# Kernel tuning notes

Hardware: AMD Instinct MI355X
Metric: run time of the kernel (lower is better)

Reference implementation:

```python
import jax, jax.numpy as jnp
import numpy as np

B, S, H, L, O = 128, 2048, 128, 2, 2  # batch, seq, hidden(=input), layers, output


def setup_inputs() -> dict:
    key = jax.random.key(0)
    k1, k2, k3, k4, k5 = jax.random.split(key, 5)
    std = 1.0 / np.sqrt(H)
    x_data = jax.random.normal(k1, (B, S, H), dtype=jnp.float32)
    x_length = jax.random.randint(k2, (B,), 0, S, dtype=jnp.int32)
    x_label = jax.random.uniform(k3, (B,), dtype=jnp.float32)
    # torch Linear layout: y = x @ W.T ; init uniform(-1/sqrt(H), 1/sqrt(H))
    Wx2h = jax.random.uniform(k4, (L, 2 * H, H), minval=-std, maxval=std, dtype=jnp.float32)
    Wfc = jax.random.uniform(k5, (L, O, H), minval=-std, maxval=std, dtype=jnp.float32)
    return {"x_data": x_data, "x_length": x_length, "x_label": x_label,
            "Wx2h": Wx2h, "Wfc": Wfc}


def reference(x_data, x_length, x_label, Wx2h, Wfc):
    Bn, Sn, Hn = x_data.shape
    Ln = Wx2h.shape[0]
    # valid-timestep mask: seq index < x_length[i]
    mask = (jnp.arange(Sn)[None, :] < x_length[:, None]).astype(x_data.dtype)  # [B,S]

    def step(carry, inp):
        S1, S2 = carry            # each [L,B,H]
        x_t, m_t = inp            # [B,H], [B]
        h = x_t
        out = None
        S1_new, S2_new = [], []
        for l in range(Ln):
            gate = h @ Wx2h[l].T                    # [B,2H]
            m1, m2 = jnp.split(gate, 2, axis=1)
            s1n = S1[l] + jnp.tanh(m1)
            s2n = S2[l] + jnp.tanh(m2)
            Fu = jax.nn.relu(s1n)
            h = (1.0 - Fu) * s2n + Fu * S2[l]       # hy
            out = jax.nn.softmax(h @ Wfc[l].T, axis=1)  # [B,O]
            S1_new.append(s1n)
            S2_new.append(s2n)
        loss_t = m_t * (x_label - jax.nn.sigmoid(out[:, 1])) ** 2  # [B]
        return (jnp.stack(S1_new), jnp.stack(S2_new)), loss_t

    S0 = jnp.zeros((Ln, Bn, Hn), x_data.dtype)
    xs = (jnp.swapaxes(x_data, 0, 1), mask.T)  # time-major [S,B,H], [S,B]
    _, losses = jax.lax.scan(step, (S0, S0), xs)
    return jnp.sum(losses)
```

## Files before the change

kernel.cpp:

```cpp
#include <hip/hip_runtime.h>

typedef __bf16 bf16;
typedef __bf16 bf16x8 __attribute__((ext_vector_type(8)));
typedef float floatx4 __attribute__((ext_vector_type(4)));

#define BATCH 128
#define SEQ   2048
#define HID   128
#define TWOH  256
#define CH    128
#define NCH   16
#define MTOT  (BATCH * SEQ)

__device__ __forceinline__ float fast_tanh(float x) {
    float e = __builtin_amdgcn_exp2f(2.88539008177793f * x);
    return 1.0f - 2.0f * __builtin_amdgcn_rcpf(e + 1.0f);
}
__device__ __forceinline__ float fast_sigmoid(float x) {
    return __builtin_amdgcn_rcpf(1.0f + __builtin_amdgcn_exp2f(-1.44269504088896f * x));
}

union PK4 { unsigned long long u; bf16 h[4]; };

__global__ __launch_bounds__(256) void convert_w_k(const float* __restrict__ W,
                                                   bf16* __restrict__ Wb) {
    int i = blockIdx.x * 256 + threadIdx.x;
    float4 v = ((const float4*)W)[i];
    PK4 pk;
    pk.h[0] = (bf16)v.x; pk.h[1] = (bf16)v.y;
    pk.h[2] = (bf16)v.z; pk.h[3] = (bf16)v.w;
    ((unsigned long long*)Wb)[i] = pk.u;
}

template <int MODE, bool AF32>
__global__ __launch_bounds__(512, 4) void fused_k(const void* __restrict__ Aptr,
                                                  const bf16* __restrict__ Wb,
                                                  const float* __restrict__ Pbase,
                                                  float* __restrict__ Pout,
                                                  bf16* __restrict__ Hb,
                                                  const float* __restrict__ Wfc,
                                                  const int* __restrict__ xlen,
                                                  const float* __restrict__ xlab,
                                                  float* __restrict__ out) {
    __shared__ bf16 As[128 * 128];
    __shared__ bf16 Bs[128 * 128];
    __shared__ float aux[512];
    __shared__ float zbuf[4][128][2];
    __shared__ float red[2];

    const int tid  = threadIdx.x;
    const int lane = tid & 63;
    const int wid  = tid >> 6;
    const int wr   = wid >> 2;
    const int wc   = wid & 3;
    const int quad = lane >> 4;
    const int l16  = lane & 15;
    const long blk = blockIdx.x;
    const long rowBase = blk * 128;

    if (AF32) {
        const float4* A4 = (const float4*)((const float*)Aptr + rowBase * HID);
        #pragma unroll
        for (int it = 0; it < 8; ++it) {
            int i  = it * 512 + tid;
            int r  = i >> 5;
            int c4 = i & 31;
            float4 v = A4[i];
            int g = c4 >> 1, hf = c4 & 1;
            PK4 pk;
            pk.h[0] = (bf16)v.x; pk.h[1] = (bf16)v.y;
            pk.h[2] = (bf16)v.z; pk.h[3] = (bf16)v.w;
            *(unsigned long long*)&As[r * 128 + ((g ^ (r & 7)) << 3) + (hf << 2)] = pk.u;
        }
    } else {
        const uint4* A8 = (const uint4*)((const bf16*)Aptr + rowBase * HID);
        #pragma unroll
        for (int it = 0; it < 4; ++it) {
            int i = it * 512 + tid;
            int r = i >> 4;
            int g = i & 15;
            uint4 v = A8[i];
            *(uint4*)&As[r * 128 + ((g ^ (r & 7)) << 3)] = v;
        }
    }

    float p1[4][2][4];

    #pragma unroll
    for (int half = 0; half < 2; ++half) {
        __syncthreads();
        {
            const uint4* W8 = (const uint4*)(Wb + half * 128 * HID);
            #pragma unroll
            for (int it = 0; it < 4; ++it) {
                int i = it * 512 + tid;
                int r = i >> 4;
                int g = i & 15;
                uint4 v = W8[i];
                *(uint4*)&Bs[r * 128 + ((g ^ (r & 7)) << 3)] = v;
            }
        }
        __syncthreads();

        floatx4 acc[4][2];
        #pragma unroll
        for (int a = 0; a < 4; ++a)
            #pragma unroll
            for (int b2 = 0; b2 < 2; ++b2) acc[a][b2] = (floatx4){0.f, 0.f, 0.f, 0.f};

        #pragma unroll
        for (int kk = 0; kk < 128; kk += 32) {
            bf16x8 af[4], bfr[2];
            int kg = (kk >> 3) + quad;
            #pragma unroll
            for (int mi = 0; mi < 4; ++mi) {
                int r = wr * 64 + mi * 16 + l16;
                af[mi] = *(const bf16x8*)&As[r * 128 + ((kg ^ (r & 7)) << 3)];
            }
            #pragma unroll
            for (int ni = 0; ni < 2; ++ni) {
                int n = wc * 32 + ni * 16 + l16;
                bfr[ni] = *(const bf16x8*)&Bs[n * 128 + ((kg ^ (n & 7)) << 3)];
            }
            #pragma unroll
            for (int mi = 0; mi < 4; ++mi)
                #pragma unroll
                for (int ni = 0; ni < 2; ++ni)
                    acc[mi][ni] = __builtin_amdgcn_mfma_f32_16x16x32_bf16(
                        af[mi], bfr[ni], acc[mi][ni], 0, 0, 0);
        }

        float g2[4][2][4];
        #pragma unroll
        for (int mi = 0; mi < 4; ++mi)
            #pragma unroll
            for (int ni = 0; ni < 2; ++ni)
                #pragma unroll
                for (int rr = 0; rr < 4; ++rr)
                    g2[mi][ni][rr] = fast_tanh(acc[mi][ni][rr]);

        if (MODE == 0) {
            #pragma unroll
            for (int ni = 0; ni < 2; ++ni) {
                float cs = 0.f;
                #pragma unroll
                for (int mi = 0; mi < 4; ++mi)
                    #pragma unroll
                    for (int rr = 0; rr < 4; ++rr) cs += g2[mi][ni][rr];
                cs += __shfl_xor(cs, 16);
                cs += __shfl_xor(cs, 32);
                if (quad == 0)
                    aux[wr * 256 + half * 128 + wc * 32 + ni * 16 + l16] = cs;
            }
        } else {
            float pref[4][2][4];
            #pragma unroll
            for (int ni = 0; ni < 2; ++ni) {
                float mibase = 0.f;
                #pragma unroll
                for (int mi = 0; mi < 4; ++mi) {
                    float s0 = g2[mi][ni][0];
                    float s1 = s0 + g2[mi][ni][1];
                    float s2 = s1 + g2[mi][ni][2];
                    float s3 = s2 + g2[mi][ni][3];
                    float tot = s3;
                    float xq = tot;
                    float t = __shfl_up(xq, 16);
                    if (quad >= 1) xq += t;
                    t = __shfl_up(xq, 32);
                    if (quad >= 2) xq += t;
                    float excl = mibase + xq - tot;
                    pref[mi][ni][0] = excl + s0;
                    pref[mi][ni][1] = excl + s1;
                    pref[mi][ni][2] = excl + s2;
                    pref[mi][ni][3] = excl + s3;
                    mibase += __shfl(xq, 48 + l16);
                }
                if (wr == 0 && quad == 0)
                    aux[wc * 32 + ni * 16 + l16] = mibase;
            }
            __syncthreads();

            if (half == 0) {
                #pragma unroll
                for (int ni = 0; ni < 2; ++ni) {
                    int col = wc * 32 + ni * 16 + l16;
                    float off = Pbase[(blk << 8) + col];
                    if (wr) off += aux[col];
                    #pragma unroll
                    for (int mi = 0; mi < 4; ++mi)
                        #pragma unroll
                        for (int rr = 0; rr < 4; ++rr)
                            p1[mi][ni][rr] = pref[mi][ni][rr] + off;
                }
            } else {
                if (MODE == 1) {
                    #pragma unroll
                    for (int ni = 0; ni < 2; ++ni) {
                        int col = wc * 32 + ni * 16 + l16;
                        float off = Pbase[(blk << 8) + 128 + col];
                        if (wr) off += aux[col];
                        #pragma unroll
                        for (int mi = 0; mi < 4; ++mi)
                            #pragma unroll
                            for (int rr = 0; rr < 4; ++rr) {
                                long row = rowBase + wr * 64 + mi * 16 + quad * 4 + rr;
                                float h = pref[mi][ni][rr] + off -
                                          fmaxf(p1[mi][ni][rr], 0.f) * g2[mi][ni][rr];
                                Hb[row * HID + col] = (bf16)h;
                            }
                    }
                } else {
                    float w0[2], w1[2], off[2];
                    #pragma unroll
                    for (int ni = 0; ni < 2; ++ni) {
                        int col = wc * 32 + ni * 16 + l16;
                        w0[ni] = Wfc[2 * HID + col];
                        w1[ni] = Wfc[3 * HID + col];
                        off[ni] = Pbase[(blk << 8) + 128 + col];
                        if (wr) off[ni] += aux[col];
                    }
                    #pragma unroll
                    for (int mi = 0; mi < 4; ++mi)
                        #pragma unroll
                        for (int rr = 0; rr < 4; ++rr) {
                            float z0 = 0.f, z1 = 0.f;
                            #pragma unroll
                            for (int ni = 0; ni < 2; ++ni) {
                                float h = pref[mi][ni][rr] + off[ni] -
                                          fmaxf(p1[mi][ni][rr], 0.f) * g2[mi][ni][rr];
                                z0 += h * w0[ni];
                                z1 += h * w1[ni];
                            }
                            z0 += __shfl_xor(z0, 1); z1 += __shfl_xor(z1, 1);
                            z0 += __shfl_xor(z0, 2); z1 += __shfl_xor(z1, 2);
                            z0 += __shfl_xor(z0, 4); z1 += __shfl_xor(z1, 4);
                            z0 += __shfl_xor(z0, 8); z1 += __shfl_xor(z1, 8);
                            if (l16 == 0) {
                                int row = wr * 64 + mi * 16 + quad * 4 + rr;
                                zbuf[wc][row][0] = z0;
                                zbuf[wc][row][1] = z1;
                            }
                        }
                }
            }
        }
    }

    if (MODE == 0) {
        __syncthreads();
        if (tid < 256) Pout[(blk << 8) + tid] = aux[tid] + aux[256 + tid];
    } else if (MODE == 2) {
        __syncthreads();
        float lsum = 0.f;
        if (tid < 128) {
            int row = tid;
            int b = (int)(blk >> 4), chunk = (int)(blk & 15);
            float z0 = zbuf[0][row][0] + zbuf[1][row][0] + zbuf[2][row][0] + zbuf[3][row][0];
            float z1 = zbuf[0][row][1] + zbuf[1][row][1] + zbuf[2][row][1] + zbuf[3][row][1];
            float o1 = fast_sigmoid(z1 - z0);
            float sg = fast_sigmoid(o1);
            float d = xlab[b] - sg;
            if (chunk * CH + row < xlen[b]) lsum = d * d;
            lsum += __shfl_xor(lsum, 1);
            lsum += __shfl_xor(lsum, 2);
            lsum += __shfl_xor(lsum, 4);
            lsum += __shfl_xor(lsum, 8);
            lsum += __shfl_xor(lsum, 16);
            lsum += __shfl_xor(lsum, 32);
            if (lane == 0) red[wid] = lsum;
        }
        __syncthreads();
        if (tid == 0) atomicAdd(out, red[0] + red[1]);
    }
}

__global__ __launch_bounds__(256) void scan_partials_k(float* __restrict__ P) {
    int ch = threadIdx.x;
    long b = blockIdx.x;
    float v[NCH];
    #pragma unroll
    for (int c = 0; c < NCH; ++c) v[c] = P[((b * NCH + c) << 8) + ch];
    float run = 0.f;
    #pragma unroll
    for (int c = 0; c < NCH; ++c) {
        float t = v[c];
        P[((b * NCH + c) << 8) + ch] = run;
        run += t;
    }
}

extern "C" void kernel_launch(void* const* d_in, const int* in_sizes, int n_in,
                              void* d_out, int out_size, void* d_ws, size_t ws_size,
                              hipStream_t stream) {
    const float* x    = (const float*)d_in[0];
    const int*   xlen = (const int*)d_in[1];
    const float* xlab = (const float*)d_in[2];
    const float* Wx2h = (const float*)d_in[3];
    const float* Wfc  = (const float*)d_in[4];
    float* out = (float*)d_out;

    char* ws = (char*)d_ws;
    bf16*  Hb = (bf16*)ws;
    float* P  = (float*)(ws + (size_t)MTOT * HID * 2);
    bf16*  Wb = (bf16*)((char*)P + (size_t)BATCH * NCH * TWOH * 4);

    hipMemsetAsync(d_out, 0, sizeof(float), stream);
    convert_w_k<<<64, 256, 0, stream>>>(Wx2h, Wb);

    fused_k<0, true><<<MTOT / 128, 512, 0, stream>>>(x, Wb, nullptr, P, nullptr,
                                                     nullptr, nullptr, nullptr, nullptr);
    scan_partials_k<<<BATCH, 256, 0, stream>>>(P);
    fused_k<1, true><<<MTOT / 128, 512, 0, stream>>>(x, Wb, P, nullptr, Hb,
                                                     nullptr, nullptr, nullptr, nullptr);
    fused_k<0, false><<<MTOT / 128, 512, 0, stream>>>(Hb, Wb + TWOH * HID, nullptr, P,
                                                      nullptr, nullptr, nullptr, nullptr, nullptr);
    scan_partials_k<<<BATCH, 256, 0, stream>>>(P);
    fused_k<2, false><<<MTOT / 128, 512, 0, stream>>>(Hb, Wb + TWOH * HID, P, nullptr,
                                                      nullptr, Wfc, xlen, xlab, out);
}
```

Baseline: 375.7 us.

## Store tanh gate tiles instead of recomputing GEMMs; fuse layer-1 input build

```diff
diff --git a/kernel.cpp b/kernel.cpp
--- a/kernel.cpp
+++ b/kernel.cpp
@@ -21,6 +21,7 @@
 }
 
 union PK4 { unsigned long long u; bf16 h[4]; };
+union PK8 { uint4 u; bf16 h[8]; };
 
 __global__ __launch_bounds__(256) void convert_w_k(const float* __restrict__ W,
                                                    bf16* __restrict__ Wb) {
@@ -32,21 +33,38 @@
     ((unsigned long long*)Wb)[i] = pk.u;
 }
 
-template <int MODE, bool AF32>
-__global__ __launch_bounds__(512, 4) void fused_k(const void* __restrict__ Aptr,
-                                                  const bf16* __restrict__ Wb,
-                                                  const float* __restrict__ Pbase,
-                                                  float* __restrict__ Pout,
-                                                  bf16* __restrict__ Hb,
-                                                  const float* __restrict__ Wfc,
-                                                  const int* __restrict__ xlen,
-                                                  const float* __restrict__ xlab,
-                                                  float* __restrict__ out) {
+__device__ __forceinline__ void tile_prefix(const float g[4][4], float pref[4][4],
+                                            float* stripe_tot, int quad, int l16) {
+    float mibase = 0.f;
+    #pragma unroll
+    for (int mi = 0; mi < 4; ++mi) {
+        float s0 = g[mi][0];
+        float s1 = s0 + g[mi][1];
+        float s2 = s1 + g[mi][2];
+        float s3 = s2 + g[mi][3];
+        float tot = s3, xq = tot;
+        float t = __shfl_up(xq, 16);
+        if (quad >= 1) xq += t;
+        t = __shfl_up(xq, 32);
+        if (quad >= 2) xq += t;
+        float excl = mibase + xq - tot;
+        pref[mi][0] = excl + s0;
+        pref[mi][1] = excl + s1;
+        pref[mi][2] = excl + s2;
+        pref[mi][3] = excl + s3;
+        mibase += __shfl(xq, 48 + l16);
+    }
+    *stripe_tot = mibase;
+}
+
+
+__global__ __launch_bounds__(512, 4) void l0_k(const float* __restrict__ x,
+                                               const bf16* __restrict__ Wb,
+                                               uint4* __restrict__ T,
+                                               float* __restrict__ Pout) {
     __shared__ bf16 As[128 * 128];
     __shared__ bf16 Bs[128 * 128];
-    __shared__ float aux[512];
-    __shared__ float zbuf[4][128][2];
-    __shared__ float red[2];
+    __shared__ float psum[512];
 
     const int tid  = threadIdx.x;
     const int lane = tid & 63;
@@ -58,8 +76,8 @@
     const long blk = blockIdx.x;
     const long rowBase = blk * 128;
 
-    if (AF32) {
-        const float4* A4 = (const float4*)((const float*)Aptr + rowBase * HID);
+    {
+        const float4* A4 = (const float4*)(x + rowBase * HID);
         #pragma unroll
         for (int it = 0; it < 8; ++it) {
             int i  = it * 512 + tid;
@@ -72,25 +90,13 @@
             pk.h[2] = (bf16)v.z; pk.h[3] = (bf16)v.w;
             *(unsigned long long*)&As[r * 128 + ((g ^ (r & 7)) << 3) + (hf << 2)] = pk.u;
         }
-    } else {
-        const uint4* A8 = (const uint4*)((const bf16*)Aptr + rowBase * HID);
-        #pragma unroll
-        for (int it = 0; it < 4; ++it) {
-            int i = it * 512 + tid;
-            int r = i >> 4;
-            int g = i & 15;
-            uint4 v = A8[i];
-            *(uint4*)&As[r * 128 + ((g ^ (r & 7)) << 3)] = v;
-        }
-    }
-
-    float p1[4][2][4];
+    }
 
     #pragma unroll
     for (int half = 0; half < 2; ++half) {
         __syncthreads();
         {
-            const uint4* W8 = (const uint4*)(Wb + half * 128 * HID);
+            const uint4* W8 = (const uint4*)(Wb + (size_t)half * 128 * HID);
             #pragma unroll
             for (int it = 0; it < 4; ++it) {
                 int i = it * 512 + tid;
@@ -130,149 +136,42 @@
                         af[mi], bfr[ni], acc[mi][ni], 0, 0, 0);
         }
 
-        float g2[4][2][4];
+        float g2[2][4][4];
         #pragma unroll
         for (int mi = 0; mi < 4; ++mi)
             #pragma unroll
             for (int ni = 0; ni < 2; ++ni)
                 #pragma unroll
                 for (int rr = 0; rr < 4; ++rr)
-                    g2[mi][ni][rr] = fast_tanh(acc[mi][ni][rr]);
-
-        if (MODE == 0) {
-            #pragma unroll
-            for (int ni = 0; ni < 2; ++ni) {
-                float cs = 0.f;
-                #pragma unroll
-                for (int mi = 0; mi < 4; ++mi)
-                    #pragma unroll
-                    for (int rr = 0; rr < 4; ++rr) cs += g2[mi][ni][rr];
-                cs += __shfl_xor(cs, 16);
-                cs += __shfl_xor(cs, 32);
-                if (quad == 0)
-                    aux[wr * 256 + half * 128 + wc * 32 + ni * 16 + l16] = cs;
-            }
-        } else {
-            float pref[4][2][4];
-            #pragma unroll
-            for (int ni = 0; ni < 2; ++ni) {
-                float mibase = 0.f;
-                #pragma unroll
-                for (int mi = 0; mi < 4; ++mi) {
-                    float s0 = g2[mi][ni][0];
-                    float s1 = s0 + g2[mi][ni][1];
-                    float s2 = s1 + g2[mi][ni][2];
-                    float s3 = s2 + g2[mi][ni][3];
-                    float tot = s3;
-                    float xq = tot;
-                    float t = __shfl_up(xq, 16);
-                    if (quad >= 1) xq += t;
-                    t = __shfl_up(xq, 32);
-                    if (quad >= 2) xq += t;
-                    float excl = mibase + xq - tot;
-                    pref[mi][ni][0] = excl + s0;
-                    pref[mi][ni][1] = excl + s1;
-                    pref[mi][ni][2] = excl + s2;
-                    pref[mi][ni][3] = excl + s3;
-                    mibase += __shfl(xq, 48 + l16);
-                }
-                if (wr == 0 && quad == 0)
-                    aux[wc * 32 + ni * 16 + l16] = mibase;
-            }
-            __syncthreads();
-
-            if (half == 0) {
-                #pragma unroll
-                for (int ni = 0; ni < 2; ++ni) {
-                    int col = wc * 32 + ni * 16 + l16;
-                    float off = Pbase[(blk << 8) + col];
-                    if (wr) off += aux[col];
-                    #pragma unroll
-                    for (int mi = 0; mi < 4; ++mi)
-                        #pragma unroll
-                        for (int rr = 0; rr < 4; ++rr)
-                            p1[mi][ni][rr] = pref[mi][ni][rr] + off;
-                }
-            } else {
-                if (MODE == 1) {
-                    #pragma unroll
-                    for (int ni = 0; ni < 2; ++ni) {
-                        int col = wc * 32 + ni * 16 + l16;
-                        float off = Pbase[(blk << 8) + 128 + col];
-                        if (wr) off += aux[col];
-                        #pragma unroll
-                        for (int mi = 0; mi < 4; ++mi)
-                            #pragma unroll
-                            for (int rr = 0; rr < 4; ++rr) {
-                                long row = rowBase + wr * 64 + mi * 16 + quad * 4 + rr;
-                                float h = pref[mi][ni][rr] + off -
-                                          fmaxf(p1[mi][ni][rr], 0.f) * g2[mi][ni][rr];
-                                Hb[row * HID + col] = (bf16)h;
-                            }
-                    }
-                } else {
-                    float w0[2], w1[2], off[2];
-                    #pragma unroll
-                    for (int ni = 0; ni < 2; ++ni) {
-                        int col = wc * 32 + ni * 16 + l16;
-                        w0[ni] = Wfc[2 * HID + col];
-                        w1[ni] = Wfc[3 * HID + col];
-                        off[ni] = Pbase[(blk << 8) + 128 + col];
-                        if (wr) off[ni] += aux[col];
-                    }
-                    #pragma unroll
-                    for (int mi = 0; mi < 4; ++mi)
-                        #pragma unroll
-                        for (int rr = 0; rr < 4; ++rr) {
-                            float z0 = 0.f, z1 = 0.f;
-                            #pragma unroll
-                            for (int ni = 0; ni < 2; ++ni) {
-                                float h = pref[mi][ni][rr] + off[ni] -
-                                          fmaxf(p1[mi][ni][rr], 0.f) * g2[mi][ni][rr];
-                                z0 += h * w0[ni];
-                                z1 += h * w1[ni];
-                            }
-                            z0 += __shfl_xor(z0, 1); z1 += __shfl_xor(z1, 1);
-                            z0 += __shfl_xor(z0, 2); z1 += __shfl_xor(z1, 2);
-                            z0 += __shfl_xor(z0, 4); z1 += __shfl_xor(z1, 4);
-                            z0 += __shfl_xor(z0, 8); z1 += __shfl_xor(z1, 8);
-                            if (l16 == 0) {
-                                int row = wr * 64 + mi * 16 + quad * 4 + rr;
-                                zbuf[wc][row][0] = z0;
-                                zbuf[wc][row][1] = z1;
-                            }
-                        }
-                }
-            }
-        }
-    }
-
-    if (MODE == 0) {
-        __syncthreads();
-        if (tid < 256) Pout[(blk << 8) + tid] = aux[tid] + aux[256 + tid];
-    } else if (MODE == 2) {
-        __syncthreads();
-        float lsum = 0.f;
-        if (tid < 128) {
-            int row = tid;
-            int b = (int)(blk >> 4), chunk = (int)(blk & 15);
-            float z0 = zbuf[0][row][0] + zbuf[1][row][0] + zbuf[2][row][0] + zbuf[3][row][0];
-            float z1 = zbuf[0][row][1] + zbuf[1][row][1] + zbuf[2][row][1] + zbuf[3][row][1];
-            float o1 = fast_sigmoid(z1 - z0);
-            float sg = fast_sigmoid(o1);
-            float d = xlab[b] - sg;
-            if (chunk * CH + row < xlen[b]) lsum = d * d;
-            lsum += __shfl_xor(lsum, 1);
-            lsum += __shfl_xor(lsum, 2);
-            lsum += __shfl_xor(lsum, 4);
-            lsum += __shfl_xor(lsum, 8);
-            lsum += __shfl_xor(lsum, 16);
-            lsum += __shfl_xor(lsum, 32);
-            if (lane == 0) red[wid] = lsum;
-        }
-        __syncthreads();
-        if (tid == 0) atomicAdd(out, red[0] + red[1]);
-    }
+                    g2[ni][mi][rr] = fast_tanh(acc[mi][ni][rr]);
+
+        #pragma unroll
+        for (int mi = 0; mi < 4; ++mi) {
+            PK8 p;
+            #pragma unroll
+            for (int rr = 0; rr < 4; ++rr) {
+                p.h[rr]     = (bf16)g2[0][mi][rr];
+                p.h[4 + rr] = (bf16)g2[1][mi][rr];
+            }
+            T[((blk * 2 + half) * 4 + mi) * 512 + tid] = p.u;
+        }
+
+        #pragma unroll
+        for (int ni = 0; ni < 2; ++ni) {
+            float cs = 0.f;
+            #pragma unroll
+            for (int mi = 0; mi < 4; ++mi)
+                #pragma unroll
+                for (int rr = 0; rr < 4; ++rr) cs += g2[ni][mi][rr];
+            cs += __shfl_xor(cs, 16);
+            cs += __shfl_xor(cs, 32);
+            if (quad == 0)
+                psum[wr * 256 + half * 128 + wc * 32 + ni * 16 + l16] = cs;
+        }
+    }
+
+    __syncthreads();
+    if (tid < 256) Pout[(blk << 8) + tid] = psum[tid] + psum[256 + tid];
 }
 
 __global__ __launch_bounds__(256) void scan_partials_k(float* __restrict__ P) {
@@ -290,6 +189,308 @@
     }
 }
 
+__global__ __launch_bounds__(512, 4) void l1_k(const bf16* __restrict__ Wb1,
+                                               uint4* __restrict__ T,
+                                               const float* __restrict__ P0,
+                                               float* __restrict__ Pout) {
+    __shared__ bf16 As[128 * 128];
+    __shared__ bf16 Bs[128 * 128];
+    __shared__ float auxp[128];
+    __shared__ float psum[512];
+
+    const int tid  = threadIdx.x;
+    const int lane = tid & 63;
+    const int wid  = tid >> 6;
+    const int wr   = wid >> 2;
+    const int wc   = wid & 3;
+    const int quad = lane >> 4;
+    const int l16  = lane & 15;
+    const long blk = blockIdx.x;
+
+    float p1[2][4][4];
+
+    {
+        float g2[2][4][4];
+        #pragma unroll
+        for (int mi = 0; mi < 4; ++mi) {
+            PK8 p;
+            p.u = T[((blk * 2 + 0) * 4 + mi) * 512 + tid];
+            #pragma unroll
+            for (int rr = 0; rr < 4; ++rr) {
+                g2[0][mi][rr] = (float)p.h[rr];
+                g2[1][mi][rr] = (float)p.h[4 + rr];
+            }
+        }
+        float pref[2][4][4], st[2];
+        #pragma unroll
+        for (int ni = 0; ni < 2; ++ni) {
+            tile_prefix(g2[ni], pref[ni], &st[ni], quad, l16);
+            if (wr == 0 && quad == 0) auxp[wc * 32 + ni * 16 + l16] = st[ni];
+        }
+        __syncthreads();
+        #pragma unroll
+        for (int ni = 0; ni < 2; ++ni) {
+            int col = wc * 32 + ni * 16 + l16;
+            float off = P0[(blk << 8) + col];
+            if (wr) off += auxp[col];
+            #pragma unroll
+            for (int mi = 0; mi < 4; ++mi)
+                #pragma unroll
+                for (int rr = 0; rr < 4; ++rr)
+                    p1[ni][mi][rr] = pref[ni][mi][rr] + off;
+        }
+    }
+    __syncthreads();
+
+    {
+        float g2[2][4][4];
+        #pragma unroll
+        for (int mi = 0; mi < 4; ++mi) {
+            PK8 p;
+            p.u = T[((blk * 2 + 1) * 4 + mi) * 512 + tid];
+            #pragma unroll
+            for (int rr = 0; rr < 4; ++rr) {
+                g2[0][mi][rr] = (float)p.h[rr];
+                g2[1][mi][rr] = (float)p.h[4 + rr];
+            }
+        }
+        float pref[2][4][4], st[2];
+        #pragma unroll
+        for (int ni = 0; ni < 2; ++ni) {
+            tile_prefix(g2[ni], pref[ni], &st[ni], quad, l16);
+            if (wr == 0 && quad == 0) auxp[wc * 32 + ni * 16 + l16] = st[ni];
+        }
+        __syncthreads();
+        #pragma unroll
+        for (int ni = 0; ni < 2; ++ni) {
+            int col = wc * 32 + ni * 16 + l16;
+            int gsw = col >> 3, rem = col & 7;
+            float off = P0[(blk << 8) + 128 + col];
+            if (wr) off += auxp[col];
+            #pragma unroll
+            for (int mi = 0; mi < 4; ++mi)
+                #pragma unroll
+                for (int rr = 0; rr < 4; ++rr) {
+                    int row = wr * 64 + mi * 16 + quad * 4 + rr;
+                    float h = pref[ni][mi][rr] + off -
+                              fmaxf(p1[ni][mi][rr], 0.f) * g2[ni][mi][rr];
+                    As[row * 128 + ((gsw ^ (row & 7)) << 3) + rem] = (bf16)h;
+                }
+        }
+    }
+
+    #pragma unroll
+    for (int half = 0; half < 2; ++half) {
+        __syncthreads();
+        {
+            const uint4* W8 = (const uint4*)(Wb1 + (size_t)half * 128 * HID);
+            #pragma unroll
+            for (int it = 0; it < 4; ++it) {
+                int i = it * 512 + tid;
+                int r = i >> 4;
+                int g = i & 15;
+                uint4 v = W8[i];
+                *(uint4*)&Bs[r * 128 + ((g ^ (r & 7)) << 3)] = v;
+            }
+        }
+        __syncthreads();
+
+        floatx4 acc[4][2];
+        #pragma unroll
+        for (int a = 0; a < 4; ++a)
+            #pragma unroll
+            for (int b2 = 0; b2 < 2; ++b2) acc[a][b2] = (floatx4){0.f, 0.f, 0.f, 0.f};
+
+        #pragma unroll
+        for (int kk = 0; kk < 128; kk += 32) {
+            bf16x8 af[4], bfr[2];
+            int kg = (kk >> 3) + quad;
+            #pragma unroll
+            for (int mi = 0; mi < 4; ++mi) {
+                int r = wr * 64 + mi * 16 + l16;
+                af[mi] = *(const bf16x8*)&As[r * 128 + ((kg ^ (r & 7)) << 3)];
+            }
+            #pragma unroll
+            for (int ni = 0; ni < 2; ++ni) {
+                int n = wc * 32 + ni * 16 + l16;
+                bfr[ni] = *(const bf16x8*)&Bs[n * 128 + ((kg ^ (n & 7)) << 3)];
+            }
+            #pragma unroll
+            for (int mi = 0; mi < 4; ++mi)
+                #pragma unroll
+                for (int ni = 0; ni < 2; ++ni)
+                    acc[mi][ni] = __builtin_amdgcn_mfma_f32_16x16x32_bf16(
+                        af[mi], bfr[ni], acc[mi][ni], 0, 0, 0);
+        }
+
+        float g2[2][4][4];
+        #pragma unroll
+        for (int mi = 0; mi < 4; ++mi)
+            #pragma unroll
+            for (int ni = 0; ni < 2; ++ni)
+                #pragma unroll
+                for (int rr = 0; rr < 4; ++rr)
+                    g2[ni][mi][rr] = fast_tanh(acc[mi][ni][rr]);
+
+        #pragma unroll
+        for (int mi = 0; mi < 4; ++mi) {
+            PK8 p;
+            #pragma unroll
+            for (int rr = 0; rr < 4; ++rr) {
+                p.h[rr]     = (bf16)g2[0][mi][rr];
+                p.h[4 + rr] = (bf16)g2[1][mi][rr];
+            }
+            T[((blk * 2 + half) * 4 + mi) * 512 + tid] = p.u;
+        }
+
+        #pragma unroll
+        for (int ni = 0; ni < 2; ++ni) {
+            float cs = 0.f;
+            #pragma unroll
+            for (int mi = 0; mi < 4; ++mi)
+                #pragma unroll
+                for (int rr = 0; rr < 4; ++rr) cs += g2[ni][mi][rr];
+            cs += __shfl_xor(cs, 16);
+            cs += __shfl_xor(cs, 32);
+            if (quad == 0)
+                psum[wr * 256 + half * 128 + wc * 32 + ni * 16 + l16] = cs;
+        }
+    }
+
+    __syncthreads();
+    if (tid < 256) Pout[(blk << 8) + tid] = psum[tid] + psum[256 + tid];
+}
+
+__global__ __launch_bounds__(512, 4) void loss_k(const uint4* __restrict__ T,
+                                                 const float* __restrict__ P1,
+                                                 const float* __restrict__ Wfc,
+                                                 const int* __restrict__ xlen,
+                                                 const float* __restrict__ xlab,
+                                                 float* __restrict__ out) {
+    __shared__ float auxp[128];
+    __shared__ float zbuf[4][128][2];
+    __shared__ float red[2];
+
+    const int tid  = threadIdx.x;
+    const int lane = tid & 63;
+    const int wid  = tid >> 6;
+    const int wr   = wid >> 2;
+    const int wc   = wid & 3;
+    const int quad = lane >> 4;
+    const int l16  = lane & 15;
+    const long blk = blockIdx.x;
+
+    float p1[2][4][4];
+
+    {
+        float g2[2][4][4];
+        #pragma unroll
+        for (int mi = 0; mi < 4; ++mi) {
+            PK8 p;
+            p.u = T[((blk * 2 + 0) * 4 + mi) * 512 + tid];
+            #pragma unroll
+            for (int rr = 0; rr < 4; ++rr) {
+                g2[0][mi][rr] = (float)p.h[rr];
+                g2[1][mi][rr] = (float)p.h[4 + rr];
+            }
+        }
+        float pref[2][4][4], st[2];
+        #pragma unroll
+        for (int ni = 0; ni < 2; ++ni) {
+            tile_prefix(g2[ni], pref[ni], &st[ni], quad, l16);
+            if (wr == 0 && quad == 0) auxp[wc * 32 + ni * 16 + l16] = st[ni];
+        }
+        __syncthreads();
+        #pragma unroll
+        for (int ni = 0; ni < 2; ++ni) {
+            int col = wc * 32 + ni * 16 + l16;
+            float off = P1[(blk << 8) + col];
+            if (wr) off += auxp[col];
+            #pragma unroll
+            for (int mi = 0; mi < 4; ++mi)
+                #pragma unroll
+                for (int rr = 0; rr < 4; ++rr)
+                    p1[ni][mi][rr] = pref[ni][mi][rr] + off;
+        }
+    }
+    __syncthreads();
+
+    {
+        float g2[2][4][4];
+        #pragma unroll
+        for (int mi = 0; mi < 4; ++mi) {
+            PK8 p;
+            p.u = T[((blk * 2 + 1) * 4 + mi) * 512 + tid];
+            #pragma unroll
+            for (int rr = 0; rr < 4; ++rr) {
+                g2[0][mi][rr] = (float)p.h[rr];
+                g2[1][mi][rr] = (float)p.h[4 + rr];
+            }
+        }
+        float pref[2][4][4], st[2];
+        #pragma unroll
+        for (int ni = 0; ni < 2; ++ni) {
+            tile_prefix(g2[ni], pref[ni], &st[ni], quad, l16);
+            if (wr == 0 && quad == 0) auxp[wc * 32 + ni * 16 + l16] = st[ni];
+        }
+        __syncthreads();
+
+        float w0[2], w1[2], off[2];
+        #pragma unroll
+        for (int ni = 0; ni < 2; ++ni) {
+            int col = wc * 32 + ni * 16 + l16;
+            w0[ni] = Wfc[2 * HID + col];
+            w1[ni] = Wfc[3 * HID + col];
+            off[ni] = P1[(blk << 8) + 128 + col];
+            if (wr) off[ni] += auxp[col];
+        }
+        #pragma unroll
+        for (int mi = 0; mi < 4; ++mi)
+            #pragma unroll
+            for (int rr = 0; rr < 4; ++rr) {
+                float z0 = 0.f, z1 = 0.f;
+                #pragma unroll
+                for (int ni = 0; ni < 2; ++ni) {
+                    float h = pref[ni][mi][rr] + off[ni] -
+                              fmaxf(p1[ni][mi][rr], 0.f) * g2[ni][mi][rr];
+                    z0 += h * w0[ni];
+                    z1 += h * w1[ni];
+                }
+                z0 += __shfl_xor(z0, 1); z1 += __shfl_xor(z1, 1);
+                z0 += __shfl_xor(z0, 2); z1 += __shfl_xor(z1, 2);
+                z0 += __shfl_xor(z0, 4); z1 += __shfl_xor(z1, 4);
+                z0 += __shfl_xor(z0, 8); z1 += __shfl_xor(z1, 8);
+                if (l16 == 0) {
+                    int row = wr * 64 + mi * 16 + quad * 4 + rr;
+                    zbuf[wc][row][0] = z0;
+                    zbuf[wc][row][1] = z1;
+                }
+            }
+    }
+
+    __syncthreads();
+    float lsum = 0.f;
+    if (tid < 128) {
+        int row = tid;
+        int b = (int)(blk >> 4), chunk = (int)(blk & 15);
+        float z0 = zbuf[0][row][0] + zbuf[1][row][0] + zbuf[2][row][0] + zbuf[3][row][0];
+        float z1 = zbuf[0][row][1] + zbuf[1][row][1] + zbuf[2][row][1] + zbuf[3][row][1];
+        float o1 = fast_sigmoid(z1 - z0);
+        float sg = fast_sigmoid(o1);
+        float d = xlab[b] - sg;
+        if (chunk * CH + row < xlen[b]) lsum = d * d;
+        lsum += __shfl_xor(lsum, 1);
+        lsum += __shfl_xor(lsum, 2);
+        lsum += __shfl_xor(lsum, 4);
+        lsum += __shfl_xor(lsum, 8);
+        lsum += __shfl_xor(lsum, 16);
+        lsum += __shfl_xor(lsum, 32);
+        if (lane == 0) red[wid] = lsum;
+    }
+    __syncthreads();
+    if (tid == 0) atomicAdd(out, red[0] + red[1]);
+}
+
 extern "C" void kernel_launch(void* const* d_in, const int* in_sizes, int n_in,
                               void* d_out, int out_size, void* d_ws, size_t ws_size,
                               hipStream_t stream) {
@@ -301,21 +502,17 @@
     float* out = (float*)d_out;
 
     char* ws = (char*)d_ws;
-    bf16*  Hb = (bf16*)ws;
-    float* P  = (float*)(ws + (size_t)MTOT * HID * 2);
-    bf16*  Wb = (bf16*)((char*)P + (size_t)BATCH * NCH * TWOH * 4);
+    uint4* T  = (uint4*)ws;
+    float* P0 = (float*)(ws + (size_t)MTOT * TWOH * 2);
+    float* P1 = P0 + (size_t)BATCH * NCH * TWOH;
+    bf16*  Wb = (bf16*)(P1 + (size_t)BATCH * NCH * TWOH);
 
     hipMemsetAsync(d_out, 0, sizeof(float), stream);
     convert_w_k<<<64, 256, 0, stream>>>(Wx2h, Wb);
 
-    fused_k<0, true><<<MTOT / 128, 512, 0, stream>>>(x, Wb, nullptr, P, nullptr,
-                                                     nullptr, nullptr, nullptr, nullptr);
-    scan_partials_k<<<BATCH, 256, 0, stream>>>(P);
-    fused_k<1, true><<<MTOT / 128, 512, 0, stream>>>(x, Wb, P, nullptr, Hb,
-                                                     nullptr, nullptr, nullptr, nullptr);
-    fused_k<0, false><<<MTOT / 128, 512, 0, stream>>>(Hb, Wb + TWOH * HID, nullptr, P,
-                                                      nullptr, nullptr, nullptr, nullptr, nullptr);
-    scan_partials_k<<<BATCH, 256, 0, stream>>>(P);
-    fused_k<2, false><<<MTOT / 128, 512, 0, stream>>>(Hb, Wb + TWOH * HID, P, nullptr,
-                                                      nullptr, Wfc, xlen, xlab, out);
-}
+    l0_k<<<MTOT / 128, 512, 0, stream>>>(x, Wb, T, P0);
+    scan_partials_k<<<BATCH, 256, 0, stream>>>(P0);
+    l1_k<<<MTOT / 128, 512, 0, stream>>>(Wb + (size_t)TWOH * HID, T, P0, P1);
+    scan_partials_k<<<BATCH, 256, 0, stream>>>(P1);
+    loss_k<<<MTOT / 128, 512, 0, stream>>>(T, P1, Wfc, xlen, xlab, out);
+}
```

Result: faster. 340.6 us (-9.3%).

## Fuse both layers into one per-batch kernel with sequential chunk scan

Applied to the files above, without the earlier changes.

```diff
diff --git a/kernel.cpp b/kernel.cpp
--- a/kernel.cpp
+++ b/kernel.cpp
@@ -10,7 +10,6 @@
 #define TWOH  256
 #define CH    128
 #define NCH   16
-#define MTOT  (BATCH * SEQ)
 
 __device__ __forceinline__ float fast_tanh(float x) {
     float e = __builtin_amdgcn_exp2f(2.88539008177793f * x);
@@ -32,19 +31,39 @@
     ((unsigned long long*)Wb)[i] = pk.u;
 }
 
-template <int MODE, bool AF32>
-__global__ __launch_bounds__(512, 4) void fused_k(const void* __restrict__ Aptr,
+__device__ __forceinline__ void tile_prefix(const float g[4][4], float pref[4][4],
+                                            float* stripe_tot, int quad, int l16) {
+    float mibase = 0.f;
+    #pragma unroll
+    for (int mi = 0; mi < 4; ++mi) {
+        float s0 = g[mi][0];
+        float s1 = s0 + g[mi][1];
+        float s2 = s1 + g[mi][2];
+        float s3 = s2 + g[mi][3];
+        float tot = s3, xq = tot;
+        float t = __shfl_up(xq, 16);
+        if (quad >= 1) xq += t;
+        t = __shfl_up(xq, 32);
+        if (quad >= 2) xq += t;
+        float excl = mibase + xq - tot;
+        pref[mi][0] = excl + s0;
+        pref[mi][1] = excl + s1;
+        pref[mi][2] = excl + s2;
+        pref[mi][3] = excl + s3;
+        mibase += __shfl(xq, 48 + l16);
+    }
+    *stripe_tot = mibase;
+}
+
+__global__ __launch_bounds__(512, 2) void batch_k(const float* __restrict__ x,
                                                   const bf16* __restrict__ Wb,
-                                                  const float* __restrict__ Pbase,
-                                                  float* __restrict__ Pout,
-                                                  bf16* __restrict__ Hb,
                                                   const float* __restrict__ Wfc,
                                                   const int* __restrict__ xlen,
                                                   const float* __restrict__ xlab,
                                                   float* __restrict__ out) {
     __shared__ bf16 As[128 * 128];
-    __shared__ bf16 Bs[128 * 128];
-    __shared__ float aux[512];
+    __shared__ bf16 Ws[256 * 128];
+    __shared__ float aux[2][2][128];
     __shared__ float zbuf[4][128][2];
     __shared__ float red[2];
 
@@ -55,171 +74,174 @@
     const int wc   = wid & 3;
     const int quad = lane >> 4;
     const int l16  = lane & 15;
-    const long blk = blockIdx.x;
-    const long rowBase = blk * 128;
-
-    if (AF32) {
-        const float4* A4 = (const float4*)((const float*)Aptr + rowBase * HID);
+    const int bb   = blockIdx.x;
+    const int xl   = xlen[bb];
+    const int nact = (xl + CH - 1) >> 7;
+    if (nact == 0) return;
+
+    float wfc0[2], wfc1[2];
+    #pragma unroll
+    for (int ni = 0; ni < 2; ++ni) {
+        int col = wc * 32 + ni * 16 + l16;
+        wfc0[ni] = Wfc[2 * HID + col];
+        wfc1[ni] = Wfc[3 * HID + col];
+    }
+    const float xlb = xlab[bb];
+
+    float offr[2][2][2];
+    #pragma unroll
+    for (int a = 0; a < 2; ++a)
+        #pragma unroll
+        for (int b = 0; b < 2; ++b) { offr[a][b][0] = 0.f; offr[a][b][1] = 0.f; }
+    float lsum = 0.f;
+
+    float4 xr[8];
+    uint4  wreg[8];
+    {
+        const float4* A4 = (const float4*)(x + (size_t)bb * SEQ * HID);
+        #pragma unroll
+        for (int it = 0; it < 8; ++it) xr[it] = A4[it * 512 + tid];
+        const uint4* W8 = (const uint4*)Wb;
+        #pragma unroll
+        for (int it = 0; it < 8; ++it) wreg[it] = W8[it * 512 + tid];
+    }
+
+    for (int c = 0; c < nact; ++c) {
+        __syncthreads();
         #pragma unroll
         for (int it = 0; it < 8; ++it) {
             int i  = it * 512 + tid;
             int r  = i >> 5;
             int c4 = i & 31;
-            float4 v = A4[i];
             int g = c4 >> 1, hf = c4 & 1;
+            float4 v = xr[it];
             PK4 pk;
             pk.h[0] = (bf16)v.x; pk.h[1] = (bf16)v.y;
             pk.h[2] = (bf16)v.z; pk.h[3] = (bf16)v.w;
             *(unsigned long long*)&As[r * 128 + ((g ^ (r & 7)) << 3) + (hf << 2)] = pk.u;
         }
-    } else {
-        const uint4* A8 = (const uint4*)((const bf16*)Aptr + rowBase * HID);
-        #pragma unroll
-        for (int it = 0; it < 4; ++it) {
+        #pragma unroll
+        for (int it = 0; it < 8; ++it) {
             int i = it * 512 + tid;
             int r = i >> 4;
             int g = i & 15;
-            uint4 v = A8[i];
-            *(uint4*)&As[r * 128 + ((g ^ (r & 7)) << 3)] = v;
-        }
-    }
-
-    float p1[4][2][4];
-
-    #pragma unroll
-    for (int half = 0; half < 2; ++half) {
+            *(uint4*)&Ws[r * 128 + ((g ^ (r & 7)) << 3)] = wreg[it];
+        }
+        if (c + 1 < nact) {
+            const float4* A4 =
+                (const float4*)(x + ((size_t)bb * SEQ + (size_t)(c + 1) * CH) * HID);
+            #pragma unroll
+            for (int it = 0; it < 8; ++it) xr[it] = A4[it * 512 + tid];
+        }
+        {
+            const uint4* W8 = (const uint4*)(Wb + (size_t)TWOH * HID);
+            #pragma unroll
+            for (int it = 0; it < 8; ++it) wreg[it] = W8[it * 512 + tid];
+        }
         __syncthreads();
-        {
-            const uint4* W8 = (const uint4*)(Wb + half * 128 * HID);
+
+        float p1[2][4][4];
+
+        #pragma unroll
+        for (int l = 0; l < 2; ++l) {
             #pragma unroll
-            for (int it = 0; it < 4; ++it) {
-                int i = it * 512 + tid;
-                int r = i >> 4;
-                int g = i & 15;
-                uint4 v = W8[i];
-                *(uint4*)&Bs[r * 128 + ((g ^ (r & 7)) << 3)] = v;
-            }
-        }
-        __syncthreads();
-
-        floatx4 acc[4][2];
-        #pragma unroll
-        for (int a = 0; a < 4; ++a)
-            #pragma unroll
-            for (int b2 = 0; b2 < 2; ++b2) acc[a][b2] = (floatx4){0.f, 0.f, 0.f, 0.f};
-
-        #pragma unroll
-        for (int kk = 0; kk < 128; kk += 32) {
-            bf16x8 af[4], bfr[2];
-            int kg = (kk >> 3) + quad;
-            #pragma unroll
-            for (int mi = 0; mi < 4; ++mi) {
-                int r = wr * 64 + mi * 16 + l16;
-                af[mi] = *(const bf16x8*)&As[r * 128 + ((kg ^ (r & 7)) << 3)];
-            }
-            #pragma unroll
-            for (int ni = 0; ni < 2; ++ni) {
-                int n = wc * 32 + ni * 16 + l16;
-                bfr[ni] = *(const bf16x8*)&Bs[n * 128 + ((kg ^ (n & 7)) << 3)];
-            }
-            #pragma unroll
-            for (int mi = 0; mi < 4; ++mi)
+            for (int h = 0; h < 2; ++h) {
+                floatx4 acc[4][2];
+                #pragma unroll
+                for (int a = 0; a < 4; ++a)
+                    #pragma unroll
+                    for (int b2 = 0; b2 < 2; ++b2)
+                        acc[a][b2] = (floatx4){0.f, 0.f, 0.f, 0.f};
+                #pragma unroll
+                for (int s = 0; s < 4; ++s) {
+                    int kg = s * 4 + quad;
+                    bf16x8 af[4], bfr[2];
+                    #pragma unroll
+                    for (int mi = 0; mi < 4; ++mi) {
+                        int r = wr * 64 + mi * 16 + l16;
+                        af[mi] = *(const bf16x8*)&As[r * 128 + ((kg ^ (r & 7)) << 3)];
+                    }
+                    #pragma unroll
+                    for (int ni = 0; ni < 2; ++ni) {
+                        int n8 = h * 128 + wc * 32 + ni * 16 + l16;
+                        bfr[ni] = *(const bf16x8*)&Ws[n8 * 128 + ((kg ^ (n8 & 7)) << 3)];
+                    }
+                    #pragma unroll
+                    for (int mi = 0; mi < 4; ++mi)
+                        #pragma unroll
+                        for (int ni = 0; ni < 2; ++ni)
+                            acc[mi][ni] = __builtin_amdgcn_mfma_f32_16x16x32_bf16(
+                                af[mi], bfr[ni], acc[mi][ni], 0, 0, 0);
+                }
+
+                float g2[2][4][4];
+                #pragma unroll
+                for (int mi = 0; mi < 4; ++mi)
+                    #pragma unroll
+                    for (int ni = 0; ni < 2; ++ni)
+                        #pragma unroll
+                        for (int rr = 0; rr < 4; ++rr)
+                            g2[ni][mi][rr] = fast_tanh(acc[mi][ni][rr]);
+
+                float pref[2][4][4], st[2];
                 #pragma unroll
                 for (int ni = 0; ni < 2; ++ni)
-                    acc[mi][ni] = __builtin_amdgcn_mfma_f32_16x16x32_bf16(
-                        af[mi], bfr[ni], acc[mi][ni], 0, 0, 0);
-        }
-
-        float g2[4][2][4];
-        #pragma unroll
-        for (int mi = 0; mi < 4; ++mi)
-            #pragma unroll
-            for (int ni = 0; ni < 2; ++ni)
-                #pragma unroll
-                for (int rr = 0; rr < 4; ++rr)
-                    g2[mi][ni][rr] = fast_tanh(acc[mi][ni][rr]);
-
-        if (MODE == 0) {
-            #pragma unroll
-            for (int ni = 0; ni < 2; ++ni) {
-                float cs = 0.f;
-                #pragma unroll
-                for (int mi = 0; mi < 4; ++mi)
-                    #pragma unroll
-                    for (int rr = 0; rr < 4; ++rr) cs += g2[mi][ni][rr];
-                cs += __shfl_xor(cs, 16);
-                cs += __shfl_xor(cs, 32);
-                if (quad == 0)
-                    aux[wr * 256 + half * 128 + wc * 32 + ni * 16 + l16] = cs;
-            }
-        } else {
-            float pref[4][2][4];
-            #pragma unroll
-            for (int ni = 0; ni < 2; ++ni) {
-                float mibase = 0.f;
-                #pragma unroll
-                for (int mi = 0; mi < 4; ++mi) {
-                    float s0 = g2[mi][ni][0];
-                    float s1 = s0 + g2[mi][ni][1];
-                    float s2 = s1 + g2[mi][ni][2];
-                    float s3 = s2 + g2[mi][ni][3];
-                    float tot = s3;
-                    float xq = tot;
-                    float t = __shfl_up(xq, 16);
-                    if (quad >= 1) xq += t;
-                    t = __shfl_up(xq, 32);
-                    if (quad >= 2) xq += t;
-                    float excl = mibase + xq - tot;
-                    pref[mi][ni][0] = excl + s0;
-                    pref[mi][ni][1] = excl + s1;
-                    pref[mi][ni][2] = excl + s2;
-                    pref[mi][ni][3] = excl + s3;
-                    mibase += __shfl(xq, 48 + l16);
+                    tile_prefix(g2[ni], pref[ni], &st[ni], quad, l16);
+                const int a = (l * 2 + h) & 1;
+                if (quad == 0) {
+                    #pragma unroll
+                    for (int ni = 0; ni < 2; ++ni)
+                        aux[a][wr][wc * 32 + ni * 16 + l16] = st[ni];
                 }
-                if (wr == 0 && quad == 0)
-                    aux[wc * 32 + ni * 16 + l16] = mibase;
-            }
-            __syncthreads();
-
-            if (half == 0) {
+                __syncthreads();
+
+                float offuse[2];
                 #pragma unroll
                 for (int ni = 0; ni < 2; ++ni) {
                     int col = wc * 32 + ni * 16 + l16;
-                    float off = Pbase[(blk << 8) + col];
-                    if (wr) off += aux[col];
-                    #pragma unroll
-                    for (int mi = 0; mi < 4; ++mi)
-                        #pragma unroll
-                        for (int rr = 0; rr < 4; ++rr)
-                            p1[mi][ni][rr] = pref[mi][ni][rr] + off;
+                    float s0t = aux[a][0][col];
+                    float tot = s0t + aux[a][1][col];
+                    offuse[ni] = offr[l][h][ni] + (wr ? s0t : 0.f);
+                    offr[l][h][ni] += tot;
                 }
-            } else {
-                if (MODE == 1) {
+
+                if (h == 0) {
+                    #pragma unroll
+                    for (int ni = 0; ni < 2; ++ni)
+                        #pragma unroll
+                        for (int mi = 0; mi < 4; ++mi)
+                            #pragma unroll
+                            for (int rr = 0; rr < 4; ++rr)
+                                p1[ni][mi][rr] = pref[ni][mi][rr] + offuse[ni];
+                } else if (l == 0) {
                     #pragma unroll
                     for (int ni = 0; ni < 2; ++ni) {
                         int col = wc * 32 + ni * 16 + l16;
-                        float off = Pbase[(blk << 8) + 128 + col];
-                        if (wr) off += aux[col];
+                        int gsw = col >> 3, rem = col & 7;
                         #pragma unroll
                         for (int mi = 0; mi < 4; ++mi)
                             #pragma unroll
                             for (int rr = 0; rr < 4; ++rr) {
-                                long row = rowBase + wr * 64 + mi * 16 + quad * 4 + rr;
-                                float h = pref[mi][ni][rr] + off -
-                                          fmaxf(p1[mi][ni][rr], 0.f) * g2[mi][ni][rr];
-                                Hb[row * HID + col] = (bf16)h;
+                                int row = wr * 64 + mi * 16 + quad * 4 + rr;
+                                float hv = pref[ni][mi][rr] + offuse[ni] -
+                                           fmaxf(p1[ni][mi][rr], 0.f) * g2[ni][mi][rr];
+                                As[row * 128 + ((gsw ^ (row & 7)) << 3) + rem] = (bf16)hv;
                             }
                     }
+                    #pragma unroll
+                    for (int it = 0; it < 8; ++it) {
+                        int i = it * 512 + tid;
+                        int r = i >> 4;
+                        int g = i & 15;
+                        *(uint4*)&Ws[r * 128 + ((g ^ (r & 7)) << 3)] = wreg[it];
+                    }
+                    if (c + 1 < nact) {
+                        const uint4* W8 = (const uint4*)Wb;
+                        #pragma unroll
+                        for (int it = 0; it < 8; ++it) wreg[it] = W8[it * 512 + tid];
+                    }
+                    __syncthreads();
                 } else {
-                    float w0[2], w1[2], off[2];
-                    #pragma unroll
-                    for (int ni = 0; ni < 2; ++ni) {
-                        int col = wc * 32 + ni * 16 + l16;
-                        w0[ni] = Wfc[2 * HID + col];
-                        w1[ni] = Wfc[3 * HID + col];
-                        off[ni] = Pbase[(blk << 8) + 128 + col];
-                        if (wr) off[ni] += aux[col];
-                    }
                     #pragma unroll
                     for (int mi = 0; mi < 4; ++mi)
                         #pragma unroll
@@ -227,10 +249,10 @@
                             float z0 = 0.f, z1 = 0.f;
                             #pragma unroll
                             for (int ni = 0; ni < 2; ++ni) {
-                                float h = pref[mi][ni][rr] + off[ni] -
-                                          fmaxf(p1[mi][ni][rr], 0.f) * g2[mi][ni][rr];
-                                z0 += h * w0[ni];
-                                z1 += h * w1[ni];
+                                float hv = pref[ni][mi][rr] + offuse[ni] -
+                                           fmaxf(p1[ni][mi][rr], 0.f) * g2[ni][mi][rr];
+                                z0 += hv * wfc0[ni];
+                                z1 += hv * wfc1[ni];
                             }
                             z0 += __shfl_xor(z0, 1); z1 += __shfl_xor(z1, 1);
                             z0 += __shfl_xor(z0, 2); z1 += __shfl_xor(z1, 2);
@@ -242,52 +264,32 @@
                                 zbuf[wc][row][1] = z1;
                             }
                         }
+                    __syncthreads();
+                    if (tid < 128) {
+                        int row = tid;
+                        float z0 = zbuf[0][row][0] + zbuf[1][row][0] +
+                                   zbuf[2][row][0] + zbuf[3][row][0];
+                        float z1 = zbuf[0][row][1] + zbuf[1][row][1] +
+                                   zbuf[2][row][1] + zbuf[3][row][1];
+                        float o1 = fast_sigmoid(z1 - z0);
+                        float sg = fast_sigmoid(o1);
+                        float d  = xlb - sg;
+                        if (c * CH + row < xl) lsum += d * d;
+                    }
                 }
             }
         }
     }
 
-    if (MODE == 0) {
-        __syncthreads();
-        if (tid < 256) Pout[(blk << 8) + tid] = aux[tid] + aux[256 + tid];
-    } else if (MODE == 2) {
-        __syncthreads();
-        float lsum = 0.f;
-        if (tid < 128) {
-            int row = tid;
-            int b = (int)(blk >> 4), chunk = (int)(blk & 15);
-            float z0 = zbuf[0][row][0] + zbuf[1][row][0] + zbuf[2][row][0] + zbuf[3][row][0];
-            float z1 = zbuf[0][row][1] + zbuf[1][row][1] + zbuf[2][row][1] + zbuf[3][row][1];
-            float o1 = fast_sigmoid(z1 - z0);
-            float sg = fast_sigmoid(o1);
-            float d = xlab[b] - sg;
-            if (chunk * CH + row < xlen[b]) lsum = d * d;
-            lsum += __shfl_xor(lsum, 1);
-            lsum += __shfl_xor(lsum, 2);
-            lsum += __shfl_xor(lsum, 4);
-            lsum += __shfl_xor(lsum, 8);
-            lsum += __shfl_xor(lsum, 16);
-            lsum += __shfl_xor(lsum, 32);
-            if (lane == 0) red[wid] = lsum;
-        }
-        __syncthreads();
-        if (tid == 0) atomicAdd(out, red[0] + red[1]);
-    }
-}
-
-__global__ __launch_bounds__(256) void scan_partials_k(float* __restrict__ P) {
-    int ch = threadIdx.x;
-    long b = blockIdx.x;
-    float v[NCH];
-    #pragma unroll
-    for (int c = 0; c < NCH; ++c) v[c] = P[((b * NCH + c) << 8) + ch];
-    float run = 0.f;
-    #pragma unroll
-    for (int c = 0; c < NCH; ++c) {
-        float t = v[c];
-        P[((b * NCH + c) << 8) + ch] = run;
-        run += t;
-    }
+    lsum += __shfl_xor(lsum, 1);
+    lsum += __shfl_xor(lsum, 2);
+    lsum += __shfl_xor(lsum, 4);
+    lsum += __shfl_xor(lsum, 8);
+    lsum += __shfl_xor(lsum, 16);
+    lsum += __shfl_xor(lsum, 32);
+    if (lane == 0 && wid < 2) red[wid] = lsum;
+    __syncthreads();
+    if (tid == 0) atomicAdd(out, red[0] + red[1]);
 }
 
 extern "C" void kernel_launch(void* const* d_in, const int* in_sizes, int n_in,
@@ -300,22 +302,9 @@
     const float* Wfc  = (const float*)d_in[4];
     float* out = (float*)d_out;
 
-    char* ws = (char*)d_ws;
-    bf16*  Hb = (bf16*)ws;
-    float* P  = (float*)(ws + (size_t)MTOT * HID * 2);
-    bf16*  Wb = (bf16*)((char*)P + (size_t)BATCH * NCH * TWOH * 4);
+    bf16* Wb = (bf16*)d_ws;
 
     hipMemsetAsync(d_out, 0, sizeof(float), stream);
     convert_w_k<<<64, 256, 0, stream>>>(Wx2h, Wb);
-
-    fused_k<0, true><<<MTOT / 128, 512, 0, stream>>>(x, Wb, nullptr, P, nullptr,
-                                                     nullptr, nullptr, nullptr, nullptr);
-    scan_partials_k<<<BATCH, 256, 0, stream>>>(P);
-    fused_k<1, true><<<MTOT / 128, 512, 0, stream>>>(x, Wb, P, nullptr, Hb,
-                                                     nullptr, nullptr, nullptr, nullptr);
-    fused_k<0, false><<<MTOT / 128, 512, 0, stream>>>(Hb, Wb + TWOH * HID, nullptr, P,
-                                                      nullptr, nullptr, nullptr, nullptr, nullptr);
-    scan_partials_k<<<BATCH, 256, 0, stream>>>(P);
-    fused_k<2, false><<<MTOT / 128, 512, 0, stream>>>(Hb, Wb + TWOH * HID, P, nullptr,
-                                                      nullptr, Wfc, xlen, xlab, out);
-}
+    batch_k<<<BATCH, 512, 0, stream>>>(x, Wb, Wfc, xlen, xlab, out);
+}
```

New measurement: 545.6 us. 1.45x slower.
